# Kernel optimization log

Hardware: AMD Instinct MI355X
Metric: run time of the kernel (lower is better)

## Reference

```python
import jax, jax.numpy as jnp
import numpy as np

N = 4096  # input_features == output_features == transform length (power of 2)


def _fft(x, twiddle_factors):
    """Faithful vectorized form of the module's radix-2 butterfly network.

    x: (N, D) complex64. twiddle_factors: (N, D) float32 (the learned weights).
    Original loop: for each stage `step`, for each block, for r in [0, half):
        k = r * (N // step)
        temp = exp(-2j*pi*k/N * twiddle_factors[k]) * x[j + half]
        new x[j + half] = x[j] - temp ; new x[j] = x[j] + temp
    Blocks are independent, so each stage is a single batched butterfly.
    """
    n = x.shape[0]
    # initial permutation: index xor with N//2 (as written in the source; not full bit-reversal)
    x = x[jnp.bitwise_xor(jnp.arange(n), n // 2)]
    step = 2
    while step <= n:  # log2(N) stages, fixed small Python loop
        half = step // 2
        k = jnp.arange(half) * (n // step)                      # (half,)
        phase = (-2.0 * jnp.pi) * (k[:, None].astype(jnp.float32) / n) * twiddle_factors[k]
        tw = jnp.exp(1j * phase)                                # (half, D) complex64
        xr = x.reshape(n // step, step, -1)                     # (blocks, step, D)
        top = xr[:, :half]
        bot = xr[:, half:]
        temp = tw[None] * bot                                   # (blocks, half, D)
        x = jnp.concatenate([top + temp, top - temp], axis=1).reshape(n, -1)
        step *= 2
    return x


def setup_inputs() -> dict:
    key = jax.random.key(0)
    kx, kw = jax.random.split(key)
    x = jax.random.normal(kx, (N, N), dtype=jnp.float32)
    weights = jax.random.normal(kw, (N, N), dtype=jnp.float32)  # nn.Parameter(randn(out, in))
    return {"x": x, "weights": weights}


def reference(x, weights):
    # input_features == output_features -> no pad / no truncation branch taken
    return _fft(x.astype(jnp.complex64), weights)
```

## Files before the change

### kernel.cpp

```cpp
#include <hip/hip_runtime.h>

#define NEG_TWOPI -6.28318530717958647692f
#define INV_N (1.0f / 4096.0f)

__device__ __forceinline__ void bf(float& ar, float& ai, float& br, float& bi,
                                   float s, float cs) {
    float tr = cs * br - s * bi;
    float ti = cs * bi + s * br;
    br = ar - tr; bi = ai - ti;
    ar = ar + tr; ai = ai + ti;
}

__device__ __forceinline__ void tw(int k, float wk, float* s, float* cs) {
    __sincosf(NEG_TWOPI * ((float)k * INV_N) * wk, s, cs);
}

__global__ __launch_bounds__(256) void fft_lo(const float* __restrict__ x,
                                              const float* __restrict__ w,
                                              float2* __restrict__ dst2,
                                              unsigned dst_lim2) {
    __shared__ __align__(16) float2 tile[64 * 64];
    const int t   = threadIdx.x;
    const int c   = t & 63;
    const int pb  = t >> 6;
    const int c0  = (blockIdx.x & 63) << 6;
    const int r0  = (blockIdx.x >> 6) << 6;
    const int src_r0 = r0 ^ 2048;
    const int col = c0 + c;

    float wp1[7];
#pragma unroll
    for (int i = 0; i < 7; ++i)
        wp1[i] = w[(size_t)(256 * (i + 1)) * 4096 + col];
    float w2a[4], w2b[8];
#pragma unroll
    for (int i = 0; i < 4; ++i)
        w2a[i] = w[(size_t)((pb + 4 * i) * 128) * 4096 + col];
#pragma unroll
    for (int i = 0; i < 8; ++i)
        w2b[i] = w[(size_t)((pb + 4 * i) * 64) * 4096 + col];

    float ar[16], ai[16];
#pragma unroll
    for (int m = 0; m < 16; ++m) {
        ar[m] = x[(size_t)(src_r0 + 16 * pb + m) * 4096 + col];
        ai[m] = 0.f;
    }

    float s1[8], c1[8];
    s1[0] = 0.f; c1[0] = 1.f;
#pragma unroll
    for (int i = 1; i < 8; ++i)
        tw(256 * i, wp1[i - 1], &s1[i], &c1[i]);

#pragma unroll
    for (int h = 1; h <= 8; h <<= 1) {
        const int step = h << 1;
#pragma unroll
        for (int r = 0; r < h; ++r) {
            const int ti = r * (8 / h);
            const float s = s1[ti], cs = c1[ti];
#pragma unroll
            for (int b = 0; b < 8 / h; ++b) {
                const int mt = b * step + r;
                bf(ar[mt], ai[mt], ar[mt + h], ai[mt + h], s, cs);
            }
        }
    }

    float s2a[4], c2a[4], s2b[8], c2b[8];
#pragma unroll
    for (int i = 0; i < 4; ++i)
        tw((pb + 4 * i) * 128, w2a[i], &s2a[i], &c2a[i]);
#pragma unroll
    for (int i = 0; i < 8; ++i)
        tw((pb + 4 * i) * 64, w2b[i], &s2b[i], &c2b[i]);

#pragma unroll
    for (int m = 0; m < 16; ++m)
        tile[(16 * pb + m) * 64 + c] = make_float2(ar[m], ai[m]);
    __syncthreads();
#pragma unroll
    for (int m = 0; m < 16; ++m) {
        float2 v = tile[(pb + 4 * m) * 64 + c];
        ar[m] = v.x; ai[m] = v.y;
    }

#pragma unroll
    for (int rm = 0; rm < 4; ++rm) {
#pragma unroll
        for (int b = 0; b < 2; ++b) {
            const int mt = b * 8 + rm;
            bf(ar[mt], ai[mt], ar[mt + 4], ai[mt + 4], s2a[rm], c2a[rm]);
        }
    }
#pragma unroll
    for (int m = 0; m < 8; ++m)
        bf(ar[m], ai[m], ar[m + 8], ai[m + 8], s2b[m], c2b[m]);

#pragma unroll
    for (int m = 0; m < 16; ++m) {
        size_t gi = (size_t)(r0 + pb + 4 * m) * 4096 + col;
        if (gi < dst_lim2) dst2[gi] = make_float2(ar[m], ai[m]);
    }
}

template <int REAL_OUT>
__global__ __launch_bounds__(256) void fft_hi(const float* __restrict__ w,
                                              const float2* __restrict__ src2,
                                              float2* __restrict__ dstc,
                                              float* __restrict__ dstr,
                                              unsigned dst_lim) {
    __shared__ __align__(16) float2 tile[64 * 64];
    const int t    = threadIdx.x;
    const int c    = t & 63;
    const int pb   = t >> 6;
    const int c0   = (blockIdx.x & 63) << 6;
    const int rres = blockIdx.x >> 6;
    const int col  = c0 + c;

    float wp1, wp2[2], wp4[4], wp8[8];
    wp1 = w[(size_t)(rres * 32) * 4096 + col];
#pragma unroll
    for (int r = 0; r < 2; ++r)
        wp2[r] = w[(size_t)((rres + 64 * r) * 16) * 4096 + col];
#pragma unroll
    for (int r = 0; r < 4; ++r)
        wp4[r] = w[(size_t)((rres + 64 * r) * 8) * 4096 + col];
#pragma unroll
    for (int r = 0; r < 8; ++r)
        wp8[r] = w[(size_t)((rres + 64 * r) * 4) * 4096 + col];
    float w2a[4], w2b[8];
#pragma unroll
    for (int i = 0; i < 4; ++i)
        w2a[i] = w[(size_t)((rres + 64 * (pb + 4 * i)) * 2) * 4096 + col];
#pragma unroll
    for (int i = 0; i < 8; ++i)
        w2b[i] = w[(size_t)(rres + 64 * (pb + 4 * i)) * 4096 + col];

    float ar[16], ai[16];
#pragma unroll
    for (int m = 0; m < 16; ++m) {
        float2 v = src2[(size_t)(rres + 64 * (16 * pb + m)) * 4096 + col];
        ar[m] = v.x; ai[m] = v.y;
    }

    {
        float s, cs;
        tw(rres * 32, wp1, &s, &cs);
#pragma unroll
        for (int b = 0; b < 8; ++b)
            bf(ar[2 * b], ai[2 * b], ar[2 * b + 1], ai[2 * b + 1], s, cs);
    }
#pragma unroll
    for (int r = 0; r < 2; ++r) {
        float s, cs;
        tw((rres + 64 * r) * 16, wp2[r], &s, &cs);
#pragma unroll
        for (int b = 0; b < 4; ++b) {
            const int mt = b * 4 + r;
            bf(ar[mt], ai[mt], ar[mt + 2], ai[mt + 2], s, cs);
        }
    }
#pragma unroll
    for (int r = 0; r < 4; ++r) {
        float s, cs;
        tw((rres + 64 * r) * 8, wp4[r], &s, &cs);
#pragma unroll
        for (int b = 0; b < 2; ++b) {
            const int mt = b * 8 + r;
            bf(ar[mt], ai[mt], ar[mt + 4], ai[mt + 4], s, cs);
        }
    }
#pragma unroll
    for (int r = 0; r < 8; ++r) {
        float s, cs;
        tw((rres + 64 * r) * 4, wp8[r], &s, &cs);
        bf(ar[r], ai[r], ar[r + 8], ai[r + 8], s, cs);
    }

    float s2a[4], c2a[4], s2b[8], c2b[8];
#pragma unroll
    for (int i = 0; i < 4; ++i)
        tw((rres + 64 * (pb + 4 * i)) * 2, w2a[i], &s2a[i], &c2a[i]);
#pragma unroll
    for (int i = 0; i < 8; ++i)
        tw(rres + 64 * (pb + 4 * i), w2b[i], &s2b[i], &c2b[i]);

#pragma unroll
    for (int m = 0; m < 16; ++m)
        tile[(16 * pb + m) * 64 + c] = make_float2(ar[m], ai[m]);
    __syncthreads();
#pragma unroll
    for (int m = 0; m < 16; ++m) {
        float2 v = tile[(pb + 4 * m) * 64 + c];
        ar[m] = v.x; ai[m] = v.y;
    }

#pragma unroll
    for (int rm = 0; rm < 4; ++rm) {
#pragma unroll
        for (int b = 0; b < 2; ++b) {
            const int mt = b * 8 + rm;
            bf(ar[mt], ai[mt], ar[mt + 4], ai[mt + 4], s2a[rm], c2a[rm]);
        }
    }
#pragma unroll
    for (int m = 0; m < 8; ++m)
        bf(ar[m], ai[m], ar[m + 8], ai[m + 8], s2b[m], c2b[m]);

    if (REAL_OUT) {
#pragma unroll
        for (int m = 0; m < 16; ++m) {
            size_t gi = (size_t)(rres + 64 * (pb + 4 * m)) * 4096 + col;
            if (gi < dst_lim) dstr[gi] = ar[m];
        }
    } else {
#pragma unroll
        for (int m = 0; m < 16; ++m) {
            size_t gi = (size_t)(rres + 64 * (pb + 4 * m)) * 4096 + col;
            if (gi < dst_lim) dstc[gi] = make_float2(ar[m], ai[m]);
        }
    }
}

extern "C" void kernel_launch(void* const* d_in, const int* in_sizes, int n_in,
                              void* d_out, int out_size, void* d_ws, size_t ws_size,
                              hipStream_t stream) {
    const float* x = (const float*)d_in[0];
    const float* w = (const float*)d_in[1];
    const long long NN = 4096LL * 4096LL;

    if ((long long)out_size >= 2 * NN) {
        float2* o2 = (float2*)d_out;
        unsigned lim2 = (unsigned)(out_size / 2);
        fft_lo<<<4096, 256, 0, stream>>>(x, w, o2, lim2);
        fft_hi<0><<<4096, 256, 0, stream>>>(w, o2, o2, nullptr, lim2);
    } else {
        float2* ws2 = (float2*)d_ws;
        unsigned ws_lim2 = (unsigned)(ws_size / 8);
        unsigned out_lim = (unsigned)out_size;
        fft_lo<<<4096, 256, 0, stream>>>(x, w, ws2, ws_lim2);
        fft_hi<1><<<4096, 256, 0, stream>>>(w, (const float2*)ws2, nullptr,
                                            (float*)d_out, out_lim);
    }
}
```

Before: 211.3 us.

## Halve shared tile via two-phase parity exchange and add nontemporal loads/stores

Replaces the single 64x64 float2 shared-memory transpose with a two-pass exchange over a 32x64 tile. Each pass moves only the register elements whose parity matches, which halves LDS use per block so more blocks can be resident, and launch_bounds now asks for 8 blocks per CU. The input x loads and the real output stores become nontemporal to reduce cache pollution. In exchange it adds one extra barrier and relies on a nontrivial index remapping that must still pair elements correctly.

```diff
diff --git a/kernel.cpp b/kernel.cpp
--- a/kernel.cpp
+++ b/kernel.cpp
@@ -15,11 +15,35 @@
     __sincosf(NEG_TWOPI * ((float)k * INV_N) * wk, s, cs);
 }
 
-__global__ __launch_bounds__(256) void fft_lo(const float* __restrict__ x,
-                                              const float* __restrict__ w,
-                                              float2* __restrict__ dst2,
-                                              unsigned dst_lim2) {
-    __shared__ __align__(16) float2 tile[64 * 64];
+__device__ __forceinline__ void exchange(float2* tile, float (&ar)[16],
+                                         float (&ai)[16], int pb, int c) {
+#pragma unroll
+    for (int par = 0; par < 2; ++par) {
+#pragma unroll
+        for (int m = 0; m < 16; ++m) {
+            if (((pb + (m >> 2) + (m & 3)) & 1) == par) {
+                int srow = (pb << 3) + (((m >> 2) << 1) | ((m & 3) >> 1));
+                tile[srow * 64 + c] = make_float2(ar[m], ai[m]);
+            }
+        }
+        __syncthreads();
+#pragma unroll
+        for (int m = 0; m < 16; ++m) {
+            if (((pb + (m >> 2) + (m & 3)) & 1) == par) {
+                int srow = ((m >> 2) << 3) + ((m & 3) << 1) + (pb >> 1);
+                float2 v = tile[srow * 64 + c];
+                ar[m] = v.x; ai[m] = v.y;
+            }
+        }
+        if (par == 0) __syncthreads();
+    }
+}
+
+__global__ __launch_bounds__(256, 8) void fft_lo(const float* __restrict__ x,
+                                                 const float* __restrict__ w,
+                                                 float2* __restrict__ dst2,
+                                                 unsigned dst_lim2) {
+    __shared__ __align__(16) float2 tile[32 * 64];
     const int t   = threadIdx.x;
     const int c   = t & 63;
     const int pb  = t >> 6;
@@ -43,7 +67,7 @@
     float ar[16], ai[16];
 #pragma unroll
     for (int m = 0; m < 16; ++m) {
-        ar[m] = x[(size_t)(src_r0 + 16 * pb + m) * 4096 + col];
+        ar[m] = __builtin_nontemporal_load(&x[(size_t)(src_r0 + 16 * pb + m) * 4096 + col]);
         ai[m] = 0.f;
     }
 
@@ -76,15 +100,7 @@
     for (int i = 0; i < 8; ++i)
         tw((pb + 4 * i) * 64, w2b[i], &s2b[i], &c2b[i]);
 
-#pragma unroll
-    for (int m = 0; m < 16; ++m)
-        tile[(16 * pb + m) * 64 + c] = make_float2(ar[m], ai[m]);
-    __syncthreads();
-#pragma unroll
-    for (int m = 0; m < 16; ++m) {
-        float2 v = tile[(pb + 4 * m) * 64 + c];
-        ar[m] = v.x; ai[m] = v.y;
-    }
+    exchange(tile, ar, ai, pb, c);
 
 #pragma unroll
     for (int rm = 0; rm < 4; ++rm) {
@@ -106,12 +122,12 @@
 }
 
 template <int REAL_OUT>
-__global__ __launch_bounds__(256) void fft_hi(const float* __restrict__ w,
-                                              const float2* __restrict__ src2,
-                                              float2* __restrict__ dstc,
-                                              float* __restrict__ dstr,
-                                              unsigned dst_lim) {
-    __shared__ __align__(16) float2 tile[64 * 64];
+__global__ __launch_bounds__(256, 8) void fft_hi(const float* __restrict__ w,
+                                                 const float2* __restrict__ src2,
+                                                 float2* __restrict__ dstc,
+                                                 float* __restrict__ dstr,
+                                                 unsigned dst_lim) {
+    __shared__ __align__(16) float2 tile[32 * 64];
     const int t    = threadIdx.x;
     const int c    = t & 63;
     const int pb   = t >> 6;
@@ -187,15 +203,7 @@
     for (int i = 0; i < 8; ++i)
         tw(rres + 64 * (pb + 4 * i), w2b[i], &s2b[i], &c2b[i]);
 
-#pragma unroll
-    for (int m = 0; m < 16; ++m)
-        tile[(16 * pb + m) * 64 + c] = make_float2(ar[m], ai[m]);
-    __syncthreads();
-#pragma unroll
-    for (int m = 0; m < 16; ++m) {
-        float2 v = tile[(pb + 4 * m) * 64 + c];
-        ar[m] = v.x; ai[m] = v.y;
-    }
+    exchange(tile, ar, ai, pb, c);
 
 #pragma unroll
     for (int rm = 0; rm < 4; ++rm) {
@@ -213,7 +221,7 @@
 #pragma unroll
         for (int m = 0; m < 16; ++m) {
             size_t gi = (size_t)(rres + 64 * (pb + 4 * m)) * 4096 + col;
-            if (gi < dst_lim) dstr[gi] = ar[m];
+            if (gi < dst_lim) __builtin_nontemporal_store(ar[m], &dstr[gi]);
         }
     } else {
 #pragma unroll
```

New measurement: 396.2 us. 1.87x slower.

## Process whole 64-point column per wavefront in registers, drop LDS exchange

Applied to the files above, without the earlier changes.

Each 64-lane wavefront now holds an entire 64-row column tile in registers (64 complex values per thread), so all six butterfly stages per kernel run without the shared-memory transpose and __syncthreads. Twiddle sincos now uses the hardware fract/sin/cos intrinsics working in revolutions. It also adds nontemporal loads and stores and cuts the grid to 1024 blocks with 4 independent tiles each. The cost is very high register pressure (128+ floats per thread, launch_bounds min 1), which may cause spills or low occupancy, and hardware sin/cos accuracy differs from __sincosf.

```diff
diff --git a/kernel.cpp b/kernel.cpp
--- a/kernel.cpp
+++ b/kernel.cpp
@@ -1,6 +1,5 @@
 #include <hip/hip_runtime.h>
 
-#define NEG_TWOPI -6.28318530717958647692f
 #define INV_N (1.0f / 4096.0f)
 
 __device__ __forceinline__ void bf(float& ar, float& ai, float& br, float& bi,
@@ -12,214 +11,125 @@
 }
 
 __device__ __forceinline__ void tw(int k, float wk, float* s, float* cs) {
-    __sincosf(NEG_TWOPI * ((float)k * INV_N) * wk, s, cs);
+    float rev = (float)k * (-INV_N) * wk;
+    rev = __builtin_amdgcn_fractf(rev);
+    *s  = __builtin_amdgcn_sinf(rev);
+    *cs = __builtin_amdgcn_cosf(rev);
 }
 
-__global__ __launch_bounds__(256) void fft_lo(const float* __restrict__ x,
-                                              const float* __restrict__ w,
-                                              float2* __restrict__ dst2,
-                                              unsigned dst_lim2) {
-    __shared__ __align__(16) float2 tile[64 * 64];
-    const int t   = threadIdx.x;
-    const int c   = t & 63;
-    const int pb  = t >> 6;
-    const int c0  = (blockIdx.x & 63) << 6;
-    const int r0  = (blockIdx.x >> 6) << 6;
+
+__global__ __launch_bounds__(256, 1) void fft_lo(const float* __restrict__ x,
+                                                 const float* __restrict__ w,
+                                                 float2* __restrict__ dst2,
+                                                 unsigned dst_lim2) {
+    const int lane = threadIdx.x & 63;
+    const int tile = (blockIdx.x << 2) + (threadIdx.x >> 6);
+    const int c0   = (tile & 63) << 6;
+    const int r0   = (tile >> 6) << 6;
     const int src_r0 = r0 ^ 2048;
-    const int col = c0 + c;
+    const unsigned col = (unsigned)(c0 + lane);
 
-    float wp1[7];
+    float ar[64], ai[64];
 #pragma unroll
-    for (int i = 0; i < 7; ++i)
-        wp1[i] = w[(size_t)(256 * (i + 1)) * 4096 + col];
-    float w2a[4], w2b[8];
-#pragma unroll
-    for (int i = 0; i < 4; ++i)
-        w2a[i] = w[(size_t)((pb + 4 * i) * 128) * 4096 + col];
-#pragma unroll
-    for (int i = 0; i < 8; ++i)
-        w2b[i] = w[(size_t)((pb + 4 * i) * 64) * 4096 + col];
-
-    float ar[16], ai[16];
-#pragma unroll
-    for (int m = 0; m < 16; ++m) {
-        ar[m] = x[(size_t)(src_r0 + 16 * pb + m) * 4096 + col];
-        ai[m] = 0.f;
+    for (int j = 0; j < 64; ++j) {
+        ar[j] = __builtin_nontemporal_load(&x[(unsigned)(src_r0 + j) * 4096u + col]);
+        ai[j] = 0.f;
     }
 
     float s1[8], c1[8];
     s1[0] = 0.f; c1[0] = 1.f;
 #pragma unroll
-    for (int i = 1; i < 8; ++i)
-        tw(256 * i, wp1[i - 1], &s1[i], &c1[i]);
-
+    for (int i = 1; i < 8; ++i) {
+        float wk = w[(unsigned)(256 * i) * 4096u + col];
+        tw(256 * i, wk, &s1[i], &c1[i]);
+    }
 #pragma unroll
     for (int h = 1; h <= 8; h <<= 1) {
-        const int step = h << 1;
 #pragma unroll
         for (int r = 0; r < h; ++r) {
             const int ti = r * (8 / h);
-            const float s = s1[ti], cs = c1[ti];
 #pragma unroll
-            for (int b = 0; b < 8 / h; ++b) {
-                const int mt = b * step + r;
-                bf(ar[mt], ai[mt], ar[mt + h], ai[mt + h], s, cs);
+            for (int b = 0; b < 32 / h; ++b) {
+                const int j = b * 2 * h + r;
+                bf(ar[j], ai[j], ar[j + h], ai[j + h], s1[ti], c1[ti]);
             }
         }
     }
 
-    float s2a[4], c2a[4], s2b[8], c2b[8];
 #pragma unroll
-    for (int i = 0; i < 4; ++i)
-        tw((pb + 4 * i) * 128, w2a[i], &s2a[i], &c2a[i]);
+    for (int r = 0; r < 16; ++r) {
+        float s = 0.f, cs = 1.f;
+        if (r) {
+            float wk = w[(unsigned)(128 * r) * 4096u + col];
+            tw(128 * r, wk, &s, &cs);
+        }
+        bf(ar[r], ai[r], ar[r + 16], ai[r + 16], s, cs);
+        bf(ar[r + 32], ai[r + 32], ar[r + 48], ai[r + 48], s, cs);
+    }
 #pragma unroll
-    for (int i = 0; i < 8; ++i)
-        tw((pb + 4 * i) * 64, w2b[i], &s2b[i], &c2b[i]);
-
-#pragma unroll
-    for (int m = 0; m < 16; ++m)
-        tile[(16 * pb + m) * 64 + c] = make_float2(ar[m], ai[m]);
-    __syncthreads();
-#pragma unroll
-    for (int m = 0; m < 16; ++m) {
-        float2 v = tile[(pb + 4 * m) * 64 + c];
-        ar[m] = v.x; ai[m] = v.y;
+    for (int r = 0; r < 32; ++r) {
+        float s = 0.f, cs = 1.f;
+        if (r) {
+            float wk = w[(unsigned)(64 * r) * 4096u + col];
+            tw(64 * r, wk, &s, &cs);
+        }
+        bf(ar[r], ai[r], ar[r + 32], ai[r + 32], s, cs);
     }
 
 #pragma unroll
-    for (int rm = 0; rm < 4; ++rm) {
-#pragma unroll
-        for (int b = 0; b < 2; ++b) {
-            const int mt = b * 8 + rm;
-            bf(ar[mt], ai[mt], ar[mt + 4], ai[mt + 4], s2a[rm], c2a[rm]);
-        }
-    }
-#pragma unroll
-    for (int m = 0; m < 8; ++m)
-        bf(ar[m], ai[m], ar[m + 8], ai[m + 8], s2b[m], c2b[m]);
-
-#pragma unroll
-    for (int m = 0; m < 16; ++m) {
-        size_t gi = (size_t)(r0 + pb + 4 * m) * 4096 + col;
-        if (gi < dst_lim2) dst2[gi] = make_float2(ar[m], ai[m]);
+    for (int j = 0; j < 64; ++j) {
+        unsigned gi = (unsigned)(r0 + j) * 4096u + col;
+        if (gi < dst_lim2) dst2[gi] = make_float2(ar[j], ai[j]);
     }
 }
 
 template <int REAL_OUT>
-__global__ __launch_bounds__(256) void fft_hi(const float* __restrict__ w,
-                                              const float2* __restrict__ src2,
-                                              float2* __restrict__ dstc,
-                                              float* __restrict__ dstr,
-                                              unsigned dst_lim) {
-    __shared__ __align__(16) float2 tile[64 * 64];
-    const int t    = threadIdx.x;
-    const int c    = t & 63;
-    const int pb   = t >> 6;
-    const int c0   = (blockIdx.x & 63) << 6;
-    const int rres = blockIdx.x >> 6;
-    const int col  = c0 + c;
+__global__ __launch_bounds__(256, 1) void fft_hi(const float* __restrict__ w,
+                                                 const float2* __restrict__ src2,
+                                                 float2* __restrict__ dstc,
+                                                 float* __restrict__ dstr,
+                                                 unsigned dst_lim) {
+    const int lane = threadIdx.x & 63;
+    const int tile = (blockIdx.x << 2) + (threadIdx.x >> 6);
+    const int cblk = tile & 63;
+    const int rres = tile >> 6;
+    const unsigned col = (unsigned)((cblk << 6) + lane);
 
-    float wp1, wp2[2], wp4[4], wp8[8];
-    wp1 = w[(size_t)(rres * 32) * 4096 + col];
+    float ar[64], ai[64];
 #pragma unroll
-    for (int r = 0; r < 2; ++r)
-        wp2[r] = w[(size_t)((rres + 64 * r) * 16) * 4096 + col];
-#pragma unroll
-    for (int r = 0; r < 4; ++r)
-        wp4[r] = w[(size_t)((rres + 64 * r) * 8) * 4096 + col];
-#pragma unroll
-    for (int r = 0; r < 8; ++r)
-        wp8[r] = w[(size_t)((rres + 64 * r) * 4) * 4096 + col];
-    float w2a[4], w2b[8];
-#pragma unroll
-    for (int i = 0; i < 4; ++i)
-        w2a[i] = w[(size_t)((rres + 64 * (pb + 4 * i)) * 2) * 4096 + col];
-#pragma unroll
-    for (int i = 0; i < 8; ++i)
-        w2b[i] = w[(size_t)(rres + 64 * (pb + 4 * i)) * 4096 + col];
-
-    float ar[16], ai[16];
-#pragma unroll
-    for (int m = 0; m < 16; ++m) {
-        float2 v = src2[(size_t)(rres + 64 * (16 * pb + m)) * 4096 + col];
-        ar[m] = v.x; ai[m] = v.y;
-    }
-
-    {
-        float s, cs;
-        tw(rres * 32, wp1, &s, &cs);
-#pragma unroll
-        for (int b = 0; b < 8; ++b)
-            bf(ar[2 * b], ai[2 * b], ar[2 * b + 1], ai[2 * b + 1], s, cs);
-    }
-#pragma unroll
-    for (int r = 0; r < 2; ++r) {
-        float s, cs;
-        tw((rres + 64 * r) * 16, wp2[r], &s, &cs);
-#pragma unroll
-        for (int b = 0; b < 4; ++b) {
-            const int mt = b * 4 + r;
-            bf(ar[mt], ai[mt], ar[mt + 2], ai[mt + 2], s, cs);
-        }
-    }
-#pragma unroll
-    for (int r = 0; r < 4; ++r) {
-        float s, cs;
-        tw((rres + 64 * r) * 8, wp4[r], &s, &cs);
-#pragma unroll
-        for (int b = 0; b < 2; ++b) {
-            const int mt = b * 8 + r;
-            bf(ar[mt], ai[mt], ar[mt + 4], ai[mt + 4], s, cs);
-        }
-    }
-#pragma unroll
-    for (int r = 0; r < 8; ++r) {
-        float s, cs;
-        tw((rres + 64 * r) * 4, wp8[r], &s, &cs);
-        bf(ar[r], ai[r], ar[r + 8], ai[r + 8], s, cs);
-    }
-
-    float s2a[4], c2a[4], s2b[8], c2b[8];
-#pragma unroll
-    for (int i = 0; i < 4; ++i)
-        tw((rres + 64 * (pb + 4 * i)) * 2, w2a[i], &s2a[i], &c2a[i]);
-#pragma unroll
-    for (int i = 0; i < 8; ++i)
-        tw(rres + 64 * (pb + 4 * i), w2b[i], &s2b[i], &c2b[i]);
-
-#pragma unroll
-    for (int m = 0; m < 16; ++m)
-        tile[(16 * pb + m) * 64 + c] = make_float2(ar[m], ai[m]);
-    __syncthreads();
-#pragma unroll
-    for (int m = 0; m < 16; ++m) {
-        float2 v = tile[(pb + 4 * m) * 64 + c];
-        ar[m] = v.x; ai[m] = v.y;
+    for (int j = 0; j < 64; ++j) {
+        float2 v = src2[(unsigned)(rres + 64 * j) * 4096u + col];
+        ar[j] = v.x; ai[j] = v.y;
     }
 
 #pragma unroll
-    for (int rm = 0; rm < 4; ++rm) {
+    for (int hl = 1; hl <= 32; hl <<= 1) {
+        const int kmul = 32 / hl;
 #pragma unroll
-        for (int b = 0; b < 2; ++b) {
-            const int mt = b * 8 + rm;
-            bf(ar[mt], ai[mt], ar[mt + 4], ai[mt + 4], s2a[rm], c2a[rm]);
+        for (int r = 0; r < hl; ++r) {
+            const int k = (rres + 64 * r) * kmul;
+            float wk = w[(unsigned)k * 4096u + col];
+            float s, cs;
+            tw(k, wk, &s, &cs);
+#pragma unroll
+            for (int b = 0; b < 32 / hl; ++b) {
+                const int j = b * 2 * hl + r;
+                bf(ar[j], ai[j], ar[j + hl], ai[j + hl], s, cs);
+            }
         }
     }
-#pragma unroll
-    for (int m = 0; m < 8; ++m)
-        bf(ar[m], ai[m], ar[m + 8], ai[m + 8], s2b[m], c2b[m]);
 
     if (REAL_OUT) {
 #pragma unroll
-        for (int m = 0; m < 16; ++m) {
-            size_t gi = (size_t)(rres + 64 * (pb + 4 * m)) * 4096 + col;
-            if (gi < dst_lim) dstr[gi] = ar[m];
+        for (int j = 0; j < 64; ++j) {
+            unsigned gi = (unsigned)(rres + 64 * j) * 4096u + col;
+            if (gi < dst_lim) __builtin_nontemporal_store(ar[j], &dstr[gi]);
         }
     } else {
 #pragma unroll
-        for (int m = 0; m < 16; ++m) {
-            size_t gi = (size_t)(rres + 64 * (pb + 4 * m)) * 4096 + col;
-            if (gi < dst_lim) dstc[gi] = make_float2(ar[m], ai[m]);
+        for (int j = 0; j < 64; ++j) {
+            unsigned gi = (unsigned)(rres + 64 * j) * 4096u + col;
+            if (gi < dst_lim) dstc[gi] = make_float2(ar[j], ai[j]);
         }
     }
 }
@@ -234,14 +144,14 @@
     if ((long long)out_size >= 2 * NN) {
         float2* o2 = (float2*)d_out;
         unsigned lim2 = (unsigned)(out_size / 2);
-        fft_lo<<<4096, 256, 0, stream>>>(x, w, o2, lim2);
-        fft_hi<0><<<4096, 256, 0, stream>>>(w, o2, o2, nullptr, lim2);
+        fft_lo<<<1024, 256, 0, stream>>>(x, w, o2, lim2);
+        fft_hi<0><<<1024, 256, 0, stream>>>(w, o2, o2, nullptr, lim2);
     } else {
         float2* ws2 = (float2*)d_ws;
         unsigned ws_lim2 = (unsigned)(ws_size / 8);
         unsigned out_lim = (unsigned)out_size;
-        fft_lo<<<4096, 256, 0, stream>>>(x, w, ws2, ws_lim2);
-        fft_hi<1><<<4096, 256, 0, stream>>>(w, (const float2*)ws2, nullptr,
+        fft_lo<<<1024, 256, 0, stream>>>(x, w, ws2, ws_lim2);
+        fft_hi<1><<<1024, 256, 0, stream>>>(w, (const float2*)ws2, nullptr,
                                             (float*)d_out, out_lim);
     }
 }
```

Measured after the change: 228.0 us. +7.9%, slower.
